# Performance work log

Hardware: AMD Instinct MI355X
Metric: run time of the kernel (lower is better)

The kernel has to match this reference:

```python
import jax, jax.numpy as jnp
import numpy as np

HIDDEN = 1024
FFN = 3584
N_EXPERTS = 8
TOP_K = 2


def setup_inputs() -> dict:
    key = jax.random.key(0)
    k1, k2, k3, k4 = jax.random.split(key, 4)
    B, S = 1, 1024
    hidden_states = jax.random.normal(k1, (B, S, HIDDEN), dtype=jnp.float32)
    gate_w = jax.random.normal(k2, (N_EXPERTS, HIDDEN), dtype=jnp.float32) * 0.02
    w_gate_up = jax.random.normal(k3, (N_EXPERTS, HIDDEN, 2 * FFN), dtype=jnp.float32) * 0.02
    w_down = jax.random.normal(k4, (N_EXPERTS, FFN, HIDDEN), dtype=jnp.float32) * 0.02
    return {"hidden_states": hidden_states, "gate_w": gate_w,
            "w_gate_up": w_gate_up, "w_down": w_down}


def reference(hidden_states, gate_w, w_gate_up, w_down):
    B, S, H = hidden_states.shape
    x = hidden_states.reshape(-1, H)                       # [T, H]
    T = x.shape[0]
    E = gate_w.shape[0]

    # Router
    router_logits = x @ gate_w.T                           # [T, E]
    probs = jax.nn.softmax(router_logits.astype(jnp.float32), axis=-1)
    routing_weights, selected = jax.lax.top_k(probs, TOP_K)  # [T, k]
    routing_weights = routing_weights / routing_weights.sum(-1, keepdims=True)

    # Dense combine matrix equivalent to permute->grouped GEMM->unpermute
    combine = jnp.zeros((T, E), probs.dtype).at[
        jnp.arange(T)[:, None], selected].add(routing_weights)  # [T, E]

    # Grouped SwiGLU expert MLPs (all experts over all tokens, masked by combine)
    gu = jnp.einsum('th,ehf->etf', x, w_gate_up)           # [E, T, 2F]
    Fdim = w_down.shape[1]
    gate_proj, up_proj = gu[..., :Fdim], gu[..., Fdim:]
    act = jax.nn.silu(gate_proj) * up_proj                 # [E, T, F]
    down = jnp.einsum('etf,efh->eth', act, w_down)         # [E, T, H]
    out = jnp.einsum('eth,te->th', down, combine.astype(down.dtype))
    return out.reshape(B, S, H), router_logits
```

## Files before the change

kernel.cpp:

```cpp
#include <hip/hip_runtime.h>
#include <hip/hip_bf16.h>
#include <math.h>

#define H 1024
#define F 3584
#define F2 7168
#define NE 8
#define T 1024

typedef __attribute__((ext_vector_type(4))) float f32x4;
typedef __attribute__((ext_vector_type(8))) short bf16x8;
typedef __attribute__((ext_vector_type(4))) short bf16x4;

__device__ inline short f2bf(float f) {
  union { float f; unsigned u; } v; v.f = f;
  unsigned r = (v.u + 0x7FFFu + ((v.u >> 16) & 1u)) >> 16;
  return (short)r;
}

__device__ inline int soff(int c, int k) {
  return ((c >> 1) << 7) + ((((c & 1) << 6) + (k << 1)) ^ (((c >> 2) & 7) << 4));
}

__global__ __launch_bounds__(64) void router_k(
    const float* __restrict__ x, const float* __restrict__ gw,
    float* __restrict__ logits, int* __restrict__ cnt,
    int* __restrict__ tok_e, int* __restrict__ tok_r, float* __restrict__ tok_w)
{
  int t = blockIdx.x, l = threadIdx.x;
  const float* xr = x + (size_t)t * H;
  double acc[NE];
  #pragma unroll
  for (int e = 0; e < NE; ++e) acc[e] = 0.0;
  for (int j = 0; j < H / 64; ++j) {
    int h = j * 64 + l;
    float xv = xr[h];
    #pragma unroll
    for (int e = 0; e < NE; ++e) acc[e] += (double)xv * (double)gw[e * H + h];
  }
  #pragma unroll
  for (int off = 32; off >= 1; off >>= 1) {
    #pragma unroll
    for (int e = 0; e < NE; ++e) acc[e] += __shfl_down(acc[e], off, 64);
  }
  if (l == 0) {
    float lg[NE];
    #pragma unroll
    for (int e = 0; e < NE; ++e) { lg[e] = (float)acc[e]; logits[t * NE + e] = lg[e]; }
    int i0 = 0;
    for (int e = 1; e < NE; ++e) if (lg[e] > lg[i0]) i0 = e;
    int i1 = (i0 == 0) ? 1 : 0;
    for (int e = 0; e < NE; ++e) if (e != i0 && lg[e] > lg[i1]) i1 = e;
    float w0 = 1.f / (1.f + expf(lg[i1] - lg[i0]));
    float w1 = 1.f / (1.f + expf(lg[i0] - lg[i1]));
    int r0 = atomicAdd(&cnt[i0], 1);
    int r1 = atomicAdd(&cnt[i1], 1);
    tok_e[2 * t] = i0;     tok_r[2 * t] = r0;     tok_w[2 * t] = w0;
    tok_e[2 * t + 1] = i1; tok_r[2 * t + 1] = r1; tok_w[2 * t + 1] = w1;
  }
}

__global__ __launch_bounds__(1024) void build_k(
    const int* __restrict__ cnt, int* __restrict__ base,
    const int* __restrict__ tok_e, const int* __restrict__ tok_r,
    const float* __restrict__ tok_w, int* __restrict__ gtok, float* __restrict__ gws)
{
  __shared__ int sb[NE];
  if (threadIdx.x == 0) {
    int s = 0;
    for (int e = 0; e < NE; ++e) { sb[e] = s; base[e] = s; s += cnt[e]; }
  }
  __syncthreads();
  int t = threadIdx.x;
  #pragma unroll
  for (int k = 0; k < 2; ++k) {
    int e = tok_e[2 * t + k];
    int slot = sb[e] + tok_r[2 * t + k];
    gtok[slot] = t;
    gws[slot] = tok_w[2 * t + k];
  }
}

__global__ __launch_bounds__(256, 3) void ffn1_k(
    const float* __restrict__ x, const float* __restrict__ wgu,
    const int* __restrict__ cnt, const int* __restrict__ base,
    const int* __restrict__ gtok, unsigned short* __restrict__ act)
{
  int wg = (blockIdx.x & 7) * 896 + (blockIdx.x >> 3);
  int mB = wg & 15;
  int ep = wg >> 4;
  int e = ep / 56, p = ep % 56;
  int n = cnt[e];
  int m0 = mB * 64;
  if (m0 >= n) return;
  int sb = base[e];
  int tid = threadIdx.x;
  int wv = tid >> 6, l = tid & 63, lr = l & 15, lg = l >> 4;

  __shared__ __align__(16) unsigned char smem[24576];
  unsigned char* sB0 = smem;
  unsigned char* sB1 = smem + 8192;
  unsigned char* sA0 = smem + 16384;
  unsigned char* sA1 = smem + 20480;

  int g = tid & 31, kg = tid >> 5;
  int tc0 = 4 * g;
  int gc = (tc0 < 64) ? (p * 64 + tc0) : (F + p * 64 + tc0 - 64);
  const float* Bg = wgu + (size_t)e * H * F2 + gc;
  int wB[4];
  #pragma unroll
  for (int j = 0; j < 4; ++j) wB[j] = soff(tc0 + j, kg * 4);

  int arow = tid & 63, aseg = tid >> 6;
  int asl = m0 + arow;
  int aslc = (asl < n) ? asl : (n - 1);
  const float* Ag = x + (size_t)gtok[sb + aslc] * H + aseg * 8;
  int wA = soff(arow, aseg * 8);

  int rA[4];
  #pragma unroll
  for (int mf = 0; mf < 4; ++mf) rA[mf] = soff(mf * 16 + lr, lg * 8);
  int rB0o = soff(wv * 16 + lr, lg * 8);
  int rB1o = soff(64 + wv * 16 + lr, lg * 8);

  f32x4 acc[4][2];
  #pragma unroll
  for (int mf = 0; mf < 4; ++mf) { acc[mf][0] = (f32x4)0.f; acc[mf][1] = (f32x4)0.f; }

  f32x4 b0[4], b1[4], a0[2], a1[2];

#define L1(S, B, A) { \
    const float* bp = Bg + (size_t)((S) * 32 + kg * 4) * F2; \
    B[0] = *(const f32x4*)bp;            B[1] = *(const f32x4*)(bp + F2); \
    B[2] = *(const f32x4*)(bp + 2 * F2); B[3] = *(const f32x4*)(bp + 3 * F2); \
    const float* ap = Ag + (S) * 32; \
    A[0] = *(const f32x4*)ap; A[1] = *(const f32x4*)(ap + 4); }

#define P1(B, A, sB, sA, SN, DO) { \
    _Pragma("unroll") for (int j = 0; j < 4; ++j) { \
      bf16x4 w; w[0] = f2bf(B[0][j]); w[1] = f2bf(B[1][j]); \
      w[2] = f2bf(B[2][j]); w[3] = f2bf(B[3][j]); \
      *(bf16x4*)((sB) + wB[j]) = w; } \
    { bf16x8 w; _Pragma("unroll") for (int i2 = 0; i2 < 4; ++i2) { \
        w[i2] = f2bf(A[0][i2]); w[4 + i2] = f2bf(A[1][i2]); } \
      *(bf16x8*)((sA) + wA) = w; } \
    asm volatile("s_waitcnt lgkmcnt(0)" ::: "memory"); \
    __builtin_amdgcn_s_barrier(); \
    if (DO) { L1(SN, B, A); } \
    bf16x8 bf0 = *(const bf16x8*)((sB) + rB0o); \
    bf16x8 bf1 = *(const bf16x8*)((sB) + rB1o); \
    _Pragma("unroll") for (int mf = 0; mf < 4; ++mf) { \
      bf16x8 af = *(const bf16x8*)((sA) + rA[mf]); \
      acc[mf][0] = __builtin_amdgcn_mfma_f32_16x16x32_bf16(af, bf0, acc[mf][0], 0, 0, 0); \
      acc[mf][1] = __builtin_amdgcn_mfma_f32_16x16x32_bf16(af, bf1, acc[mf][1], 0, 0, 0); } }

  L1(0, b0, a0);
  L1(1, b1, a1);

  for (int it = 0; it < 16; ++it) {
    int s = 2 * it;
    bool more = (it < 15);
    P1(b0, a0, sB0, sA0, s + 2, more);
    P1(b1, a1, sB1, sA1, s + 3, more);
  }
#undef L1
#undef P1

  int fcol = p * 64 + wv * 16 + lr;
  #pragma unroll
  for (int mf = 0; mf < 4; ++mf) {
    #pragma unroll
    for (int r = 0; r < 4; ++r) {
      int sl = m0 + mf * 16 + lg * 4 + r;
      if (sl < n) {
        float gg = acc[mf][0][r], u = acc[mf][1][r];
        act[(size_t)(sb + sl) * F + fcol] = (unsigned short)f2bf(gg / (1.f + expf(-gg)) * u);
      }
    }
  }
}

__global__ __launch_bounds__(256, 3) void ffn2_k(
    const unsigned short* __restrict__ act, const float* __restrict__ wd,
    const int* __restrict__ cnt, const int* __restrict__ base,
    const int* __restrict__ gtok, const float* __restrict__ gws,
    float* __restrict__ out)
{
  int wg = (blockIdx.x & 7) * 256 + (blockIdx.x >> 3);
  int mB = wg & 15;
  int r2 = wg >> 4;
  int p = r2 & 7;
  int ekh = r2 >> 3;
  int kh = ekh & 1, e = ekh >> 1;
  int n = cnt[e];
  int m0 = mB * 64;
  if (m0 >= n) return;
  int sb = base[e];
  int tid = threadIdx.x;
  int wv = tid >> 6, l = tid & 63, lr = l & 15, lg = l >> 4;
  const int kbase = kh * 1792;

  __shared__ __align__(16) unsigned char smem[24576];
  unsigned char* sB0 = smem;
  unsigned char* sB1 = smem + 8192;
  unsigned char* sA0 = smem + 16384;
  unsigned char* sA1 = smem + 20480;

  int g = tid & 31, kg = tid >> 5;
  int tc0 = 4 * g;
  const float* Bg = wd + (size_t)e * F * H + (size_t)kbase * H + p * 128 + tc0;
  int wB[4];
  #pragma unroll
  for (int j = 0; j < 4; ++j) wB[j] = soff(tc0 + j, kg * 4);

  int arow = tid & 63, aseg = tid >> 6;
  int asl = m0 + arow;
  int aslc = (asl < n) ? asl : (n - 1);
  const unsigned short* Ag = act + (size_t)(sb + aslc) * F + kbase + aseg * 8;
  int wA = soff(arow, aseg * 8);

  int rA[4];
  #pragma unroll
  for (int mf = 0; mf < 4; ++mf) rA[mf] = soff(mf * 16 + lr, lg * 8);
  int rB0o = soff(wv * 16 + lr, lg * 8);
  int rB1o = soff(64 + wv * 16 + lr, lg * 8);

  f32x4 acc[4][2];
  #pragma unroll
  for (int mf = 0; mf < 4; ++mf) { acc[mf][0] = (f32x4)0.f; acc[mf][1] = (f32x4)0.f; }

  f32x4 b0[4], b1[4];
  bf16x8 a0, a1;

#define L2K(S, B, A) { \
    const float* bp = Bg + (size_t)((S) * 32 + kg * 4) * H; \
    B[0] = *(const f32x4*)bp;           B[1] = *(const f32x4*)(bp + H); \
    B[2] = *(const f32x4*)(bp + 2 * H); B[3] = *(const f32x4*)(bp + 3 * H); \
    A = *(const bf16x8*)(Ag + (S) * 32); }

#define P2(B, A, sB, sA, SN, DO) { \
    _Pragma("unroll") for (int j = 0; j < 4; ++j) { \
      bf16x4 w; w[0] = f2bf(B[0][j]); w[1] = f2bf(B[1][j]); \
      w[2] = f2bf(B[2][j]); w[3] = f2bf(B[3][j]); \
      *(bf16x4*)((sB) + wB[j]) = w; } \
    *(bf16x8*)((sA) + wA) = A; \
    asm volatile("s_waitcnt lgkmcnt(0)" ::: "memory"); \
    __builtin_amdgcn_s_barrier(); \
    if (DO) { L2K(SN, B, A); } \
    bf16x8 bf0 = *(const bf16x8*)((sB) + rB0o); \
    bf16x8 bf1 = *(const bf16x8*)((sB) + rB1o); \
    _Pragma("unroll") for (int mf = 0; mf < 4; ++mf) { \
      bf16x8 af = *(const bf16x8*)((sA) + rA[mf]); \
      acc[mf][0] = __builtin_amdgcn_mfma_f32_16x16x32_bf16(af, bf0, acc[mf][0], 0, 0, 0); \
      acc[mf][1] = __builtin_amdgcn_mfma_f32_16x16x32_bf16(af, bf1, acc[mf][1], 0, 0, 0); } }

  L2K(0, b0, a0);
  L2K(1, b1, a1);

  for (int it = 0; it < 28; ++it) {
    int s = 2 * it;
    bool more = (it < 27);
    P2(b0, a0, sB0, sA0, s + 2, more);
    P2(b1, a1, sB1, sA1, s + 3, more);
  }
#undef L2K
#undef P2

  #pragma unroll
  for (int mf = 0; mf < 4; ++mf) {
    #pragma unroll
    for (int r = 0; r < 4; ++r) {
      int sl = m0 + mf * 16 + lg * 4 + r;
      if (sl < n) {
        int slot = sb + sl;
        int tok = gtok[slot];
        float w = gws[slot];
        atomicAdd(&out[(size_t)tok * H + p * 128 + wv * 16 + lr], w * acc[mf][0][r]);
        atomicAdd(&out[(size_t)tok * H + p * 128 + 64 + wv * 16 + lr], w * acc[mf][1][r]);
      }
    }
  }
}

extern "C" void kernel_launch(void* const* d_in, const int* in_sizes, int n_in,
                              void* d_out, int out_size, void* d_ws, size_t ws_size,
                              hipStream_t stream)
{
  const float* x   = (const float*)d_in[0];
  const float* gw  = (const float*)d_in[1];
  const float* wgu = (const float*)d_in[2];
  const float* wdn = (const float*)d_in[3];
  float* out = (float*)d_out;
  float* logits = out + (size_t)T * H;

  char* w = (char*)d_ws;
  int*   cnt = (int*)(w);
  int*   bs  = (int*)(w + 32);
  int*   te  = (int*)(w + 64);
  int*   tr  = (int*)(w + 64 + 8192);
  float* tw  = (float*)(w + 64 + 16384);
  int*   gt  = (int*)(w + 64 + 24576);
  float* gwt = (float*)(w + 64 + 32768);
  unsigned short* act = (unsigned short*)(w + 65536);

  hipMemsetAsync(d_out, 0, (size_t)T * H * sizeof(float), stream);
  hipMemsetAsync(cnt, 0, NE * sizeof(int), stream);
  router_k<<<T, 64, 0, stream>>>(x, gw, logits, cnt, te, tr, tw);
  build_k<<<1, 1024, 0, stream>>>(cnt, bs, te, tr, tw, gt, gwt);
  ffn1_k<<<7168, 256, 0, stream>>>(x, wgu, cnt, bs, gt, act);
  ffn2_k<<<2048, 256, 0, stream>>>(act, wdn, cnt, bs, gt, gwt, out);
}
```

Before: 319.3 us.

## Triple-buffer FFN GEMM pipelines and use packed bf16 conversion instruction

```diff
diff --git a/kernel.cpp b/kernel.cpp
--- a/kernel.cpp
+++ b/kernel.cpp
@@ -10,12 +10,19 @@
 
 typedef __attribute__((ext_vector_type(4))) float f32x4;
 typedef __attribute__((ext_vector_type(8))) short bf16x8;
-typedef __attribute__((ext_vector_type(4))) short bf16x4;
+typedef __attribute__((ext_vector_type(2))) unsigned u32x2;
+typedef __attribute__((ext_vector_type(4))) unsigned u32x4;
 
 __device__ inline short f2bf(float f) {
   union { float f; unsigned u; } v; v.f = f;
   unsigned r = (v.u + 0x7FFFu + ((v.u >> 16) & 1u)) >> 16;
   return (short)r;
+}
+
+__device__ inline unsigned pkbf(float a, float b) {
+  unsigned r;
+  asm("v_cvt_pk_bf16_f32 %0, %1, %2" : "=v"(r) : "v"(a), "v"(b));
+  return r;
 }
 
 __device__ inline int soff(int c, int k) {
@@ -97,11 +104,13 @@
   int tid = threadIdx.x;
   int wv = tid >> 6, l = tid & 63, lr = l & 15, lg = l >> 4;
 
-  __shared__ __align__(16) unsigned char smem[24576];
+  __shared__ __align__(16) unsigned char smem[36864];
   unsigned char* sB0 = smem;
   unsigned char* sB1 = smem + 8192;
-  unsigned char* sA0 = smem + 16384;
-  unsigned char* sA1 = smem + 20480;
+  unsigned char* sB2 = smem + 16384;
+  unsigned char* sA0 = smem + 24576;
+  unsigned char* sA1 = smem + 28672;
+  unsigned char* sA2 = smem + 32768;
 
   int g = tid & 31, kg = tid >> 5;
   int tc0 = 4 * g;
@@ -127,7 +136,7 @@
   #pragma unroll
   for (int mf = 0; mf < 4; ++mf) { acc[mf][0] = (f32x4)0.f; acc[mf][1] = (f32x4)0.f; }
 
-  f32x4 b0[4], b1[4], a0[2], a1[2];
+  f32x4 b0[4], b1[4], b2[4], a0[2], a1[2], a2[2];
 
 #define L1(S, B, A) { \
     const float* bp = Bg + (size_t)((S) * 32 + kg * 4) * F2; \
@@ -138,15 +147,14 @@
 
 #define P1(B, A, sB, sA, SN, DO) { \
     _Pragma("unroll") for (int j = 0; j < 4; ++j) { \
-      bf16x4 w; w[0] = f2bf(B[0][j]); w[1] = f2bf(B[1][j]); \
-      w[2] = f2bf(B[2][j]); w[3] = f2bf(B[3][j]); \
-      *(bf16x4*)((sB) + wB[j]) = w; } \
-    { bf16x8 w; _Pragma("unroll") for (int i2 = 0; i2 < 4; ++i2) { \
-        w[i2] = f2bf(A[0][i2]); w[4 + i2] = f2bf(A[1][i2]); } \
-      *(bf16x8*)((sA) + wA) = w; } \
+      u32x2 w; w[0] = pkbf(B[0][j], B[1][j]); w[1] = pkbf(B[2][j], B[3][j]); \
+      *(u32x2*)((sB) + wB[j]) = w; } \
+    { u32x4 w; w[0] = pkbf(A[0][0], A[0][1]); w[1] = pkbf(A[0][2], A[0][3]); \
+      w[2] = pkbf(A[1][0], A[1][1]); w[3] = pkbf(A[1][2], A[1][3]); \
+      *(u32x4*)((sA) + wA) = w; } \
+    if (DO) { L1(SN, B, A); } \
     asm volatile("s_waitcnt lgkmcnt(0)" ::: "memory"); \
     __builtin_amdgcn_s_barrier(); \
-    if (DO) { L1(SN, B, A); } \
     bf16x8 bf0 = *(const bf16x8*)((sB) + rB0o); \
     bf16x8 bf1 = *(const bf16x8*)((sB) + rB1o); \
     _Pragma("unroll") for (int mf = 0; mf < 4; ++mf) { \
@@ -156,13 +164,16 @@
 
   L1(0, b0, a0);
   L1(1, b1, a1);
-
-  for (int it = 0; it < 16; ++it) {
-    int s = 2 * it;
-    bool more = (it < 15);
-    P1(b0, a0, sB0, sA0, s + 2, more);
-    P1(b1, a1, sB1, sA1, s + 3, more);
-  }
+  L1(2, b2, a2);
+
+  for (int it = 0; it < 10; ++it) {
+    int s = 3 * it;
+    P1(b0, a0, sB0, sA0, s + 3, true);
+    P1(b1, a1, sB1, sA1, s + 4, true);
+    P1(b2, a2, sB2, sA2, s + 5, (it < 9));
+  }
+  P1(b0, a0, sB0, sA0, 0, false);
+  P1(b1, a1, sB1, sA1, 0, false);
 #undef L1
 #undef P1
 
@@ -200,11 +211,13 @@
   int wv = tid >> 6, l = tid & 63, lr = l & 15, lg = l >> 4;
   const int kbase = kh * 1792;
 
-  __shared__ __align__(16) unsigned char smem[24576];
+  __shared__ __align__(16) unsigned char smem[36864];
   unsigned char* sB0 = smem;
   unsigned char* sB1 = smem + 8192;
-  unsigned char* sA0 = smem + 16384;
-  unsigned char* sA1 = smem + 20480;
+  unsigned char* sB2 = smem + 16384;
+  unsigned char* sA0 = smem + 24576;
+  unsigned char* sA1 = smem + 28672;
+  unsigned char* sA2 = smem + 32768;
 
   int g = tid & 31, kg = tid >> 5;
   int tc0 = 4 * g;
@@ -229,8 +242,8 @@
   #pragma unroll
   for (int mf = 0; mf < 4; ++mf) { acc[mf][0] = (f32x4)0.f; acc[mf][1] = (f32x4)0.f; }
 
-  f32x4 b0[4], b1[4];
-  bf16x8 a0, a1;
+  f32x4 b0[4], b1[4], b2[4];
+  bf16x8 a0, a1, a2;
 
 #define L2K(S, B, A) { \
     const float* bp = Bg + (size_t)((S) * 32 + kg * 4) * H; \
@@ -240,13 +253,12 @@
 
 #define P2(B, A, sB, sA, SN, DO) { \
     _Pragma("unroll") for (int j = 0; j < 4; ++j) { \
-      bf16x4 w; w[0] = f2bf(B[0][j]); w[1] = f2bf(B[1][j]); \
-      w[2] = f2bf(B[2][j]); w[3] = f2bf(B[3][j]); \
-      *(bf16x4*)((sB) + wB[j]) = w; } \
+      u32x2 w; w[0] = pkbf(B[0][j], B[1][j]); w[1] = pkbf(B[2][j], B[3][j]); \
+      *(u32x2*)((sB) + wB[j]) = w; } \
     *(bf16x8*)((sA) + wA) = A; \
+    if (DO) { L2K(SN, B, A); } \
     asm volatile("s_waitcnt lgkmcnt(0)" ::: "memory"); \
     __builtin_amdgcn_s_barrier(); \
-    if (DO) { L2K(SN, B, A); } \
     bf16x8 bf0 = *(const bf16x8*)((sB) + rB0o); \
     bf16x8 bf1 = *(const bf16x8*)((sB) + rB1o); \
     _Pragma("unroll") for (int mf = 0; mf < 4; ++mf) { \
@@ -256,13 +268,16 @@
 
   L2K(0, b0, a0);
   L2K(1, b1, a1);
-
-  for (int it = 0; it < 28; ++it) {
-    int s = 2 * it;
-    bool more = (it < 27);
-    P2(b0, a0, sB0, sA0, s + 2, more);
-    P2(b1, a1, sB1, sA1, s + 3, more);
-  }
+  L2K(2, b2, a2);
+
+  for (int it = 0; it < 18; ++it) {
+    int s = 3 * it;
+    P2(b0, a0, sB0, sA0, s + 3, true);
+    P2(b1, a1, sB1, sA1, s + 4, true);
+    P2(b2, a2, sB2, sA2, s + 5, (it < 17));
+  }
+  P2(b0, a0, sB0, sA0, 0, false);
+  P2(b1, a1, sB1, sA1, 0, false);
 #undef L2K
 #undef P2
 
```

Measured after the change: 295.6 us. 7.4% less time.
